# Optimization experiments

Measured on AMD Instinct MI355X. Metric: run time of the kernel, lower is better.

## Reference

```python
import jax, jax.numpy as jnp
import numpy as np

BS, H, W, A, NC, G = 2048, 14, 14, 5, 2, 30
SIZE = 1 + NC + 4  # conf, classes, x, y, w, h
OBJ_SCALE, NOOBJ_SCALE, CLASS_SCALE, COORD_SCALE = 5.0, 0.5, 1.0, 1.0


def setup_inputs() -> dict:
    key = jax.random.key(0)
    pred = jax.random.normal(key, (BS, A * SIZE, H, W), dtype=jnp.float32) * 0.5
    # Structured label: G ground-truth boxes per image at distinct cells.
    rng = np.random.default_rng(0)
    lab = np.zeros((BS, 7, H, W), np.float32)
    perm = np.argsort(rng.random((BS, H * W)), axis=1)[:, :G]  # distinct cells
    r, c = perm // W, perm % W
    b = np.arange(BS)[:, None]
    lab[b, 0, r, c] = 1.0
    cls = rng.integers(0, 2, (BS, G)).astype(np.float32)
    lab[b, 1, r, c] = cls
    lab[b, 2, r, c] = 1.0 - cls
    lab[b, 3, r, c] = rng.uniform(0.1, 0.9, (BS, G))  # tx in-cell offset
    lab[b, 4, r, c] = rng.uniform(0.1, 0.9, (BS, G))  # ty
    lab[b, 5, r, c] = rng.uniform(0.05, 0.4, (BS, G))  # tw (normalized)
    lab[b, 6, r, c] = rng.uniform(0.05, 0.4, (BS, G))  # th
    anchors = np.array([[42.0, 44.0], [91.0, 104.0], [162.0, 220.0],
                        [299.0, 170.0], [396.0, 359.0]], np.float32)
    return {"pred": pred, "label": jnp.asarray(lab),
            "anchors": jnp.asarray(anchors), "seen": 6400}


def _yolo_v2_loss(pred, label, anchors, seen):
    f32 = jnp.float32
    anchor_bias = anchors / (512.0 / 14.0) / jnp.array([W, H], f32)  # [A,2], grid-normalized
    # [BS,H,W,A,SIZE]
    pred_r = pred.transpose(0, 2, 3, 1).reshape(BS, H, W, A, SIZE)
    sxy = jax.nn.sigmoid(pred_r[..., 1 + NC:3 + NC])               # sigmoid(x,y)
    ids = jnp.stack(jnp.meshgrid(jnp.arange(W, dtype=f32),
                                 jnp.arange(H, dtype=f32)), -1)[:, :, None, :]  # [H,W,1,2]=(c,r)
    coords = (sxy + ids) / jnp.array([W, H], f32)                  # normalized centers
    wh = jnp.exp(pred_r[..., 3 + NC:5 + NC]) * anchor_bias         # normalized w,h
    boxes = jnp.concatenate([coords, wh], -1)                      # [BS,H,W,A,4]
    aw, ah = anchor_bias[:, 0], anchor_bias[:, 1]

    def per_image(pred_b, sxy_b, boxes_b, label_b):
        obj = label_b[0].reshape(-1)
        vals, flat = jax.lax.top_k(obj, G)
        valid = vals > 0                                           # [G]
        r = flat // W
        c = flat % W
        tx, ty = label_b[3, r, c], label_b[4, r, c]
        tw = jnp.where(valid, label_b[5, r, c], 1.0)
        th = jnp.where(valid, label_b[6, r, c], 1.0)
        # gt boxes are built from detached .data in the torch code -> stop_gradient
        gx = jax.lax.stop_gradient((tx + c.astype(f32)) / W)
        gy = jax.lax.stop_gradient((ty + r.astype(f32)) / H)
        tw = jax.lax.stop_gradient(tw)
        th = jax.lax.stop_gradient(th)
        # pairwise IoU pred boxes [H,W,A] vs gt [G] -> [H,W,A,G]
        x1, y1 = boxes_b[..., 0:1], boxes_b[..., 1:2]
        w1, h1 = boxes_b[..., 2:3], boxes_b[..., 3:4]
        xi1 = jnp.maximum(x1 - 0.5 * w1, gx - 0.5 * tw)
        yi1 = jnp.maximum(y1 - 0.5 * h1, gy - 0.5 * th)
        xi2 = jnp.minimum(x1 + 0.5 * w1, gx + 0.5 * tw)
        yi2 = jnp.minimum(y1 + 0.5 * h1, gy + 0.5 * th)
        inter = jnp.maximum(xi2 - xi1, 0.0) * jnp.maximum(yi2 - yi1, 0.0)
        union = w1 * h1 + tw * th - inter
        iou = jnp.maximum(inter / union, 0.0)
        iou = jnp.where(valid, iou, 0.0)
        noobj = (iou.max(-1) <= 0.6).astype(f32) * (NOOBJ_SCALE * pred_b[..., 0])
        if seen < 12800:
            prior = 0.01 * jnp.concatenate([sxy_b - 0.5,
                                            pred_b[..., 3 + NC:5 + NC]], -1)
        else:
            prior = jnp.zeros((H, W, A, 4), f32)
        coord_obj = jnp.concatenate([prior, noobj[..., None]], -1)  # [H,W,A,5]
        # best anchor per gt (IoU of (0,0,tw,th) vs (0,0,aw,ah))
        ia = jnp.minimum(tw[:, None], aw) * jnp.minimum(th[:, None], ah)
        aid = jnp.argmax(ia / (tw[:, None] * th[:, None] + aw * ah - ia), axis=1)
        wi = (gx * W).astype(jnp.int32)
        fx = gx * W - wi.astype(f32)
        hj = (gy * H).astype(jnp.int32)
        fy = gy * H - hj.astype(f32)
        twh = jnp.log(jnp.stack([tw, th], 1) / anchor_bias[aid])    # [G,2]
        truth_coords = jnp.concatenate([fx[:, None], fy[:, None], twh], 1)
        p_sel = pred_b[hj, wi, aid]                                 # [G,SIZE]
        pc = jnp.concatenate([sxy_b[hj, wi, aid], p_sel[:, 3 + NC:5 + NC]], 1)
        wgt = COORD_SCALE * (2.0 - fx * fy)                         # detached in torch
        closs = wgt[:, None] * (pc - truth_coords)                  # [G,4]
        iou_sel = iou[hj, wi, aid, jnp.arange(G)]                   # [G]
        objl = OBJ_SCALE * (p_sel[:, 0] - iou_sel)
        tco = jnp.concatenate([closs, objl[:, None]], 1) * valid[:, None].astype(f32)
        cvec = jnp.stack([label_b[1, hj, wi], label_b[2, hj, wi]], 1)
        cls_l = CLASS_SCALE * (p_sel[:, 1:1 + NC] - cvec)
        loss_cls = jnp.sum((cls_l ** 2) * valid[:, None].astype(f32))
        m = jnp.zeros((H, W, A), f32).at[hj, wi, aid].add(valid.astype(f32))
        ta = jnp.zeros((H, W, A, 5), f32).at[hj, wi, aid].add(tco)
        m4 = m[..., None]
        comb = m4 * ta + (1.0 - m4) * coord_obj
        il = loss_cls + jnp.sum(comb ** 2)
        return jnp.where(jnp.any(valid), il, 0.0)

    losses = jax.vmap(per_image)(pred_r, sxy, boxes, label)
    return jnp.reshape(jnp.sum(losses) / BS, (1,))


def reference(pred, label, anchors, seen):
    return _yolo_v2_loss(pred, label, anchors, seen)
```

## Files before the change

kernel.cpp:

```cpp
#include <hip/hip_runtime.h>
#include <math.h>

#define BS 2048
#define H_ 14
#define W_ 14
#define A_ 5
#define G_ 30
#define HW_ 196
#define NCELL 980
#define NTHREADS 256
#define LABN (7 * HW_)
#define LAB4 (LABN / 4)

__device__ __forceinline__ float fast_rcp(float x) { return __builtin_amdgcn_rcpf(x); }

__global__ __launch_bounds__(NTHREADS) void yolo_main(
    const float* __restrict__ pred,
    const float* __restrict__ label,
    const float* __restrict__ anchors,
    float* __restrict__ partial)
{
    __shared__ float  s_lab[LABN];
    __shared__ float4 s_box[G_];
    __shared__ float  s_thr[G_];
    __shared__ float  s_area[G_];
    __shared__ float4 s_tgt[G_];
    __shared__ float4 s_aux[G_];
    __shared__ float  s_aw[A_], s_ah[A_];
    __shared__ short  s_map[NCELL];
    __shared__ int    s_flat[G_];
    __shared__ int    s_wcnt[NTHREADS / 64];
    __shared__ float  s_red[NTHREADS / 64];

    const int b    = blockIdx.x;
    const int tid  = threadIdx.x;
    const int lane = tid & 63;
    const int wv   = tid >> 6;
    const float* lb = label + (size_t)b * LABN;
    const float* pb = pred  + (size_t)b * (A_ * 7 * HW_);

    {
        const float4* l4 = (const float4*)lb;
        float4* s4 = (float4*)s_lab;
        for (int i = tid; i < LAB4; i += NTHREADS) s4[i] = l4[i];
    }
    for (int i = tid; i < NCELL; i += NTHREADS) s_map[i] = -1;
    if (tid < A_) {
        const float div1 = 512.0f / 14.0f;
        s_aw[tid] = anchors[2 * tid]     / div1 / (float)W_;
        s_ah[tid] = anchors[2 * tid + 1] / div1 / (float)H_;
    }
    __syncthreads();

    float objv = (tid < HW_) ? s_lab[tid] : 0.0f;
    unsigned long long bm = __ballot(objv > 0.0f);
    if (lane == 0) s_wcnt[wv] = __popcll(bm);
    __syncthreads();
    if (objv > 0.0f) {
        int rank = __popcll(bm & ((1ULL << lane) - 1ULL));
        for (int w2 = 0; w2 < wv; ++w2) rank += s_wcnt[w2];
        s_flat[rank] = tid;
    }
    __syncthreads();

    if (tid < G_) {
        int flat = s_flat[tid];
        int r = flat / W_, c = flat - r * W_;
        float tx = s_lab[3 * HW_ + flat];
        float ty = s_lab[4 * HW_ + flat];
        float tw = s_lab[5 * HW_ + flat];
        float th = s_lab[6 * HW_ + flat];
        float gx = (tx + (float)c) / (float)W_;
        float gy = (ty + (float)r) / (float)H_;
        int   wi = (int)(gx * (float)W_);
        int   hj = (int)(gy * (float)H_);
        float fx = gx * (float)W_ - (float)wi;
        float fy = gy * (float)H_ - (float)hj;
        float best = -1.0f; int aid = 0;
        for (int a = 0; a < A_; ++a) {
            float ia = fminf(tw, s_aw[a]) * fminf(th, s_ah[a]);
            float m  = ia / (tw * th + s_aw[a] * s_ah[a] - ia);
            if (m > best) { best = m; aid = a; }
        }
        s_box[tid]  = make_float4(gx - 0.5f * tw, gy - 0.5f * th,
                                  gx + 0.5f * tw, gy + 0.5f * th);
        s_area[tid] = tw * th;
        s_thr[tid]  = 0.375f * tw * th;
        s_tgt[tid]  = make_float4(fx, fy, logf(tw / s_aw[aid]), logf(th / s_ah[aid]));
        s_aux[tid]  = make_float4(2.0f - fx * fy,
                                  s_lab[1 * HW_ + hj * W_ + wi],
                                  s_lab[2 * HW_ + hj * W_ + wi],
                                  0.0f);
        s_map[(hj * W_ + wi) * A_ + aid] = (short)tid;
    }
    __syncthreads();

    float lsum = 0.0f;
    if (tid < 245) {
        int a   = tid / 49;
        int q   = tid - a * 49;
        int hw0 = 4 * q;
        const float4* p4 = (const float4*)(pb + a * 7 * HW_);
        float4 P0 = p4[0 * 49 + q];
        float4 P1 = p4[1 * 49 + q];
        float4 P2 = p4[2 * 49 + q];
        float4 P3 = p4[3 * 49 + q];
        float4 P4 = p4[4 * 49 + q];
        float4 P5 = p4[5 * 49 + q];
        float4 P6 = p4[6 * 49 + q];
        float p0v[4] = {P0.x, P0.y, P0.z, P0.w};
        float p1v[4] = {P1.x, P1.y, P1.z, P1.w};
        float p2v[4] = {P2.x, P2.y, P2.z, P2.w};
        float p3v[4] = {P3.x, P3.y, P3.z, P3.w};
        float p4v[4] = {P4.x, P4.y, P4.z, P4.w};
        float p5v[4] = {P5.x, P5.y, P5.z, P5.w};
        float p6v[4] = {P6.x, P6.y, P6.z, P6.w};

        float aw = s_aw[a], ah = s_ah[a];
        float sxv[4], syv[4], xlo[4], xhi[4], ylo[4], yhi[4], acc[4];
        #pragma unroll
        for (int j = 0; j < 4; ++j) {
            int hw = hw0 + j;
            int h  = hw / W_;
            int w  = hw - h * W_;
            float sx = fast_rcp(1.0f + __expf(-p3v[j]));
            float sy = fast_rcp(1.0f + __expf(-p4v[j]));
            float bw = __expf(p5v[j]) * aw;
            float bh = __expf(p6v[j]) * ah;
            float x1 = (sx + (float)w) * (1.0f / (float)W_);
            float y1 = (sy + (float)h) * (1.0f / (float)H_);
            sxv[j] = sx;  syv[j] = sy;
            xlo[j] = x1 - 0.5f * bw;  xhi[j] = x1 + 0.5f * bw;
            ylo[j] = y1 - 0.5f * bh;  yhi[j] = y1 + 0.5f * bh;
            acc[j] = -1e30f;
        }

        #pragma unroll 5
        for (int g = 0; g < G_; ++g) {
            float4 bx  = s_box[g];
            float  thr = s_thr[g];
            #pragma unroll
            for (int j = 0; j < 4; ++j) {
                float xi1 = fmaxf(xlo[j], bx.x);
                float yi1 = fmaxf(ylo[j], bx.y);
                float xi2 = fminf(xhi[j], bx.z);
                float yi2 = fminf(yhi[j], bx.w);
                float dx = fmaxf(xi2 - xi1, 0.0f);
                float dy = fmaxf(yi2 - yi1, 0.0f);
                acc[j] = fmaxf(acc[j], fmaf(dx, dy, -thr));
            }
        }

        #pragma unroll
        for (int j = 0; j < 4; ++j) {
            int g_at = s_map[(hw0 + j) * A_ + a];
            float area1 = (xhi[j] - xlo[j]) * (yhi[j] - ylo[j]);
            if (g_at >= 0) {
                float4 t  = s_tgt[g_at];
                float4 u  = s_aux[g_at];
                float4 bx = s_box[g_at];
                float xi1 = fmaxf(xlo[j], bx.x);
                float yi1 = fmaxf(ylo[j], bx.y);
                float xi2 = fminf(xhi[j], bx.z);
                float yi2 = fminf(yhi[j], bx.w);
                float inter = fmaxf(xi2 - xi1, 0.0f) * fmaxf(yi2 - yi1, 0.0f);
                float uni   = area1 + s_area[g_at] - inter;
                float iou   = fmaxf(inter * fast_rcp(uni), 0.0f);
                float wg = u.x;
                float d0 = wg * (sxv[j] - t.x);
                float d1 = wg * (syv[j] - t.y);
                float d2 = wg * (p5v[j] - t.z);
                float d3 = wg * (p6v[j] - t.w);
                float ob = 5.0f * (p0v[j] - iou);
                float c1 = p1v[j] - u.y;
                float c2 = p2v[j] - u.z;
                lsum += d0*d0 + d1*d1 + d2*d2 + d3*d3 + ob*ob + c1*c1 + c2*c2;
            } else {
                float pr0 = 0.01f * (sxv[j] - 0.5f);
                float pr1 = 0.01f * (syv[j] - 0.5f);
                float pr2 = 0.01f * p5v[j];
                float pr3 = 0.01f * p6v[j];
                float no  = (acc[j] <= 0.375f * area1) ? 0.5f * p0v[j] : 0.0f;
                lsum += pr0*pr0 + pr1*pr1 + pr2*pr2 + pr3*pr3 + no*no;
            }
        }
    }

    #pragma unroll
    for (int off = 32; off > 0; off >>= 1)
        lsum += __shfl_down(lsum, off, 64);
    if (lane == 0) s_red[wv] = lsum;
    __syncthreads();
    if (tid == 0) {
        float tot = 0.0f;
        #pragma unroll
        for (int i = 0; i < NTHREADS / 64; ++i) tot += s_red[i];
        partial[b] = tot;
    }
}

__global__ __launch_bounds__(NTHREADS) void yolo_reduce(
    const float* __restrict__ partial, float* __restrict__ out)
{
    __shared__ float s_red[NTHREADS / 64];
    const int tid = threadIdx.x, lane = tid & 63, wv = tid >> 6;
    float s = 0.0f;
    for (int i = tid; i < BS; i += NTHREADS) s += partial[i];
    #pragma unroll
    for (int off = 32; off > 0; off >>= 1)
        s += __shfl_down(s, off, 64);
    if (lane == 0) s_red[wv] = s;
    __syncthreads();
    if (tid == 0) {
        float tot = 0.0f;
        #pragma unroll
        for (int i = 0; i < NTHREADS / 64; ++i) tot += s_red[i];
        out[0] = tot * (1.0f / (float)BS);
    }
}

extern "C" void kernel_launch(void* const* d_in, const int* in_sizes, int n_in,
                              void* d_out, int out_size, void* d_ws, size_t ws_size,
                              hipStream_t stream) {
    const float* pred    = (const float*)d_in[0];
    const float* label   = (const float*)d_in[1];
    const float* anchors = (const float*)d_in[2];
    float* out     = (float*)d_out;
    float* partial = (float*)d_ws;

    yolo_main<<<dim3(BS), dim3(NTHREADS), 0, stream>>>(pred, label, anchors, partial);
    yolo_reduce<<<dim3(1), dim3(NTHREADS), 0, stream>>>(partial, out);
}
```

Before: 115.3 us.

## Prefetch predictions early, drop a barrier, and fuse final reduction via atomics

Issues the per-thread prediction loads and reads the objectness directly from global memory at kernel start, so their latency overlaps the label staging and gt-box setup. This also removes one __syncthreads. Replaces the separate reduction kernel with a per-block atomicAdd into the output, which is zeroed by a memset beforehand. It also switches logf to __logf. In exchange, float atomic ordering makes the sum nondeterministic, the memset adds a launch, and more registers stay live across the setup phase.

```diff
diff --git a/kernel.cpp b/kernel.cpp
--- a/kernel.cpp
+++ b/kernel.cpp
@@ -18,7 +18,7 @@
     const float* __restrict__ pred,
     const float* __restrict__ label,
     const float* __restrict__ anchors,
-    float* __restrict__ partial)
+    float* __restrict__ out)
 {
     __shared__ float  s_lab[LABN];
     __shared__ float4 s_box[G_];
@@ -39,6 +39,24 @@
     const float* lb = label + (size_t)b * LABN;
     const float* pb = pred  + (size_t)b * (A_ * 7 * HW_);
 
+    const bool active = tid < 245;
+    int a = 0, q = 0;
+    float4 P0, P1, P2, P3, P4, P5, P6;
+    P0 = P1 = P2 = P3 = P4 = P5 = P6 = make_float4(0.f, 0.f, 0.f, 0.f);
+    if (active) {
+        a = tid / 49;
+        q = tid - a * 49;
+        const float4* p4 = (const float4*)(pb + a * 7 * HW_);
+        P0 = p4[0 * 49 + q];
+        P1 = p4[1 * 49 + q];
+        P2 = p4[2 * 49 + q];
+        P3 = p4[3 * 49 + q];
+        P4 = p4[4 * 49 + q];
+        P5 = p4[5 * 49 + q];
+        P6 = p4[6 * 49 + q];
+    }
+    float objv = (tid < HW_) ? lb[tid] : 0.0f;
+
     {
         const float4* l4 = (const float4*)lb;
         float4* s4 = (float4*)s_lab;
@@ -50,9 +68,7 @@
         s_aw[tid] = anchors[2 * tid]     / div1 / (float)W_;
         s_ah[tid] = anchors[2 * tid + 1] / div1 / (float)H_;
     }
-    __syncthreads();
-
-    float objv = (tid < HW_) ? s_lab[tid] : 0.0f;
+
     unsigned long long bm = __ballot(objv > 0.0f);
     if (lane == 0) s_wcnt[wv] = __popcll(bm);
     __syncthreads();
@@ -77,16 +93,16 @@
         float fx = gx * (float)W_ - (float)wi;
         float fy = gy * (float)H_ - (float)hj;
         float best = -1.0f; int aid = 0;
-        for (int a = 0; a < A_; ++a) {
-            float ia = fminf(tw, s_aw[a]) * fminf(th, s_ah[a]);
-            float m  = ia / (tw * th + s_aw[a] * s_ah[a] - ia);
-            if (m > best) { best = m; aid = a; }
+        for (int aa = 0; aa < A_; ++aa) {
+            float ia = fminf(tw, s_aw[aa]) * fminf(th, s_ah[aa]);
+            float m  = ia / (tw * th + s_aw[aa] * s_ah[aa] - ia);
+            if (m > best) { best = m; aid = aa; }
         }
         s_box[tid]  = make_float4(gx - 0.5f * tw, gy - 0.5f * th,
                                   gx + 0.5f * tw, gy + 0.5f * th);
         s_area[tid] = tw * th;
         s_thr[tid]  = 0.375f * tw * th;
-        s_tgt[tid]  = make_float4(fx, fy, logf(tw / s_aw[aid]), logf(th / s_ah[aid]));
+        s_tgt[tid]  = make_float4(fx, fy, __logf(tw / s_aw[aid]), __logf(th / s_ah[aid]));
         s_aux[tid]  = make_float4(2.0f - fx * fy,
                                   s_lab[1 * HW_ + hj * W_ + wi],
                                   s_lab[2 * HW_ + hj * W_ + wi],
@@ -96,18 +112,8 @@
     __syncthreads();
 
     float lsum = 0.0f;
-    if (tid < 245) {
-        int a   = tid / 49;
-        int q   = tid - a * 49;
+    if (active) {
         int hw0 = 4 * q;
-        const float4* p4 = (const float4*)(pb + a * 7 * HW_);
-        float4 P0 = p4[0 * 49 + q];
-        float4 P1 = p4[1 * 49 + q];
-        float4 P2 = p4[2 * 49 + q];
-        float4 P3 = p4[3 * 49 + q];
-        float4 P4 = p4[4 * 49 + q];
-        float4 P5 = p4[5 * 49 + q];
-        float4 P6 = p4[6 * 49 + q];
         float p0v[4] = {P0.x, P0.y, P0.z, P0.w};
         float p1v[4] = {P1.x, P1.y, P1.z, P1.w};
         float p2v[4] = {P2.x, P2.y, P2.z, P2.w};
@@ -195,27 +201,7 @@
         float tot = 0.0f;
         #pragma unroll
         for (int i = 0; i < NTHREADS / 64; ++i) tot += s_red[i];
-        partial[b] = tot;
-    }
-}
-
-__global__ __launch_bounds__(NTHREADS) void yolo_reduce(
-    const float* __restrict__ partial, float* __restrict__ out)
-{
-    __shared__ float s_red[NTHREADS / 64];
-    const int tid = threadIdx.x, lane = tid & 63, wv = tid >> 6;
-    float s = 0.0f;
-    for (int i = tid; i < BS; i += NTHREADS) s += partial[i];
-    #pragma unroll
-    for (int off = 32; off > 0; off >>= 1)
-        s += __shfl_down(s, off, 64);
-    if (lane == 0) s_red[wv] = s;
-    __syncthreads();
-    if (tid == 0) {
-        float tot = 0.0f;
-        #pragma unroll
-        for (int i = 0; i < NTHREADS / 64; ++i) tot += s_red[i];
-        out[0] = tot * (1.0f / (float)BS);
+        atomicAdd(out, tot * (1.0f / (float)BS));
     }
 }
 
@@ -225,9 +211,8 @@
     const float* pred    = (const float*)d_in[0];
     const float* label   = (const float*)d_in[1];
     const float* anchors = (const float*)d_in[2];
-    float* out     = (float*)d_out;
-    float* partial = (float*)d_ws;
-
-    yolo_main<<<dim3(BS), dim3(NTHREADS), 0, stream>>>(pred, label, anchors, partial);
-    yolo_reduce<<<dim3(1), dim3(NTHREADS), 0, stream>>>(partial, out);
+    float* out = (float*)d_out;
+
+    hipMemsetAsync(out, 0, sizeof(float), stream);
+    yolo_main<<<dim3(BS), dim3(NTHREADS), 0, stream>>>(pred, label, anchors, out);
 }
```

New measurement: 125.2 us. 1.09x slower.
